# Kernel optimization log

Measured on AMD Instinct MI355X. Metric: run time of the kernel, lower is better.

The kernel has to match this reference:

```python
import jax, jax.numpy as jnp
import numpy as np

B, I, H, O = 64, 2048, 2048, 2048


def setup_inputs() -> dict:
    key = jax.random.key(0)
    ks = jax.random.split(key, 17)
    s = 0.02  # keep activations in a sane range
    return {
        "x": jax.random.normal(ks[0], (B, I), jnp.float32),
        "h_prev": jax.random.normal(ks[1], (B, H), jnp.float32),
        "c_prev": jax.random.normal(ks[2], (B, H), jnp.float32),
        "Wfh": jax.random.normal(ks[3], (H, H), jnp.float32) * s,
        "Wfx": jax.random.normal(ks[4], (I, H), jnp.float32) * s,
        "bf": jax.random.normal(ks[5], (H,), jnp.float32) * s,
        "Wih": jax.random.normal(ks[6], (H, H), jnp.float32) * s,
        "Wix": jax.random.normal(ks[7], (I, H), jnp.float32) * s,
        "bi": jax.random.normal(ks[8], (H,), jnp.float32) * s,
        "Woh": jax.random.normal(ks[9], (H, H), jnp.float32) * s,
        "Wox": jax.random.normal(ks[10], (I, H), jnp.float32) * s,
        "bo": jax.random.normal(ks[11], (H,), jnp.float32) * s,
        "Wch": jax.random.normal(ks[12], (H, H), jnp.float32) * s,
        "Wcx": jax.random.normal(ks[13], (I, H), jnp.float32) * s,
        "bc": jax.random.normal(ks[14], (H,), jnp.float32) * s,
        "Wy": jax.random.normal(ks[15], (H, O), jnp.float32) * s,
        "by": jax.random.normal(ks[16], (O,), jnp.float32) * s,
    }


def reference(x, h_prev, c_prev, Wfh, Wfx, bf, Wih, Wix, bi,
              Woh, Wox, bo, Wch, Wcx, bc, Wy, by):
    # Fused single-step LSTM cell: concat the 4 per-gate matmuls into
    # two GEMMs ([B,H]@[H,4H] and [B,I]@[I,4H]) -- same math as the
    # original 8 separate matmuls, gate order (f, i, c~, o).
    Wh = jnp.concatenate([Wfh, Wih, Wch, Woh], axis=1)  # [H, 4H]
    Wx = jnp.concatenate([Wfx, Wix, Wcx, Wox], axis=1)  # [I, 4H]
    b = jnp.concatenate([bf, bi, bc, bo], axis=0)       # [4H]
    gates = h_prev @ Wh + x @ Wx + b                     # [B, 4H]
    f_, i_, ct_, o_ = jnp.split(gates, 4, axis=1)
    f = jax.nn.sigmoid(f_)
    i = jax.nn.sigmoid(i_)
    ct = jnp.tanh(ct_)
    o = jax.nn.sigmoid(o_)
    c = f * c_prev + i * ct
    h = o * jnp.tanh(c)
    # NOTE: original computes y from the PREVIOUS hidden state (hList[-1])
    y = h_prev @ Wy + by
    # Pack (y, h_new, c_new) along feature dim (O == H) for a single output.
    return jnp.concatenate([y, h, c], axis=-1)  # [B, O + 2H]
```

## Files before the change

### kernel.cpp

```cpp
#include <hip/hip_runtime.h>

#define GAS __attribute__((address_space(1)))
#define LAS __attribute__((address_space(3)))

typedef short  bf16x8  __attribute__((ext_vector_type(8)));
typedef float  f32x4   __attribute__((ext_vector_type(4)));
typedef float  f32x16  __attribute__((ext_vector_type(16)));
typedef unsigned short ushort;

__device__ __forceinline__ short f2bf(float f) {
  __bf16 h = (__bf16)f;
  return __builtin_bit_cast(short, h);
}

#define GATE_PART 0
#define Y_PART    4194304
#define ABF_OFF   5242880

__global__ __launch_bounds__(256) void lstm_aconv(
    const float* __restrict__ X, const float* __restrict__ H,
    ushort* __restrict__ Abf)
{
  const int t  = blockIdx.x * 256 + threadIdx.x;
  const int e0 = t * 8;
  const int b  = e0 >> 12;
  const int k  = e0 & 4095;
  const float* src = (k < 2048) ? (H + (size_t)b * 2048 + k)
                                : (X + (size_t)b * 2048 + (k - 2048));
  f32x4 v0 = *(const f32x4*)(src);
  f32x4 v1 = *(const f32x4*)(src + 4);
  bf16x8 o;
  o[0] = f2bf(v0[0]); o[1] = f2bf(v0[1]); o[2] = f2bf(v0[2]); o[3] = f2bf(v0[3]);
  o[4] = f2bf(v1[0]); o[5] = f2bf(v1[1]); o[6] = f2bf(v1[2]); o[7] = f2bf(v1[3]);
  *(bf16x8*)(Abf + e0) = o;
}

__global__ __launch_bounds__(256, 2) void lstm_gemm(
    const float* __restrict__ Wfh, const float* __restrict__ Wfx, const float* __restrict__ bfp,
    const float* __restrict__ Wih, const float* __restrict__ Wix, const float* __restrict__ bip,
    const float* __restrict__ Woh, const float* __restrict__ Wox, const float* __restrict__ bop,
    const float* __restrict__ Wch, const float* __restrict__ Wcx, const float* __restrict__ bcp,
    const float* __restrict__ Wy,  const float* __restrict__ by,
    float* __restrict__ ws)
{
  __shared__ float  ldsW[2][64 * 128];
  __shared__ ushort ldsA[2][64 * 64];

  const int tid  = threadIdx.x;
  const int lane = tid & 63;
  const int widx = tid >> 6;
  const int n    = lane & 31;
  const int kg8  = (lane >> 5) << 3;
  const int j0w  = widx * 32;
  const ushort* Abf = (const ushort*)(ws + ABF_OFF);

  const int bid = blockIdx.x;
  const float* Wmat; int krow0m, aK0, nch;
  float bias; float* outBase; int outStride;

  if (bid < 512) {
    const int gate   = bid >> 7;
    const int stripe = (bid >> 3) & 15;
    const int ks     = bid & 7;
    const int j0     = stripe * 128;
    const float *Wg_h, *Wg_x, *bg;
    if      (gate == 0) { Wg_h = Wfh; Wg_x = Wfx; bg = bfp; }
    else if (gate == 1) { Wg_h = Wih; Wg_x = Wix; bg = bip; }
    else if (gate == 2) { Wg_h = Wch; Wg_x = Wcx; bg = bcp; }
    else                { Wg_h = Woh; Wg_x = Wox; bg = bop; }
    Wmat    = ((ks < 4) ? Wg_h : Wg_x) + j0;
    krow0m  = (ks & 3) * 512;
    aK0     = ks * 512;
    nch     = 8;
    bias    = (ks == 0) ? bg[j0 + j0w + n] : 0.f;
    outBase = ws + GATE_PART + (size_t)ks * 524288 + (size_t)gate * 2048 + j0 + j0w + n;
    outStride = 8192;
  } else {
    const int yi     = bid - 512;
    const int stripe = yi >> 3;
    const int ksy    = yi & 7;
    const int j0     = stripe * 128;
    Wmat    = Wy + j0;
    krow0m  = ksy * 256;
    aK0     = krow0m;
    nch     = 4;
    bias    = (ksy == 0) ? by[j0 + j0w + n] : 0.f;
    outBase = ws + Y_PART + (size_t)ksy * 131072 + j0 + j0w + n;
    outStride = 2048;
  }

  auto stageW = [&](int buf, int krow) {
    #pragma unroll
    for (int i = 0; i < 8; ++i) {
      const int r = i * 8 + widx * 2 + (lane >> 5);
      const float* src = Wmat + (size_t)(krow + r) * 2048 + (lane & 31) * 4;
      float* dst = &ldsW[buf][(i * 8 + widx * 2) * 128];
      __builtin_amdgcn_global_load_lds((const GAS unsigned*)src,
                                       (LAS unsigned*)dst, 16, 0, 0);
    }
  };
  auto stageA = [&](int buf, int aK) {
    #pragma unroll
    for (int i = 0; i < 2; ++i) {
      const int b    = i * 32 + widx * 8 + (lane >> 3);
      const int coff = (((lane & 7) * 16) ^ ((b & 7) << 4)) >> 1;
      const ushort* src = Abf + (size_t)b * 4096 + aK + coff;
      ushort* dst = &ldsA[buf][(i * 32 + widx * 8) * 64];
      __builtin_amdgcn_global_load_lds((const GAS unsigned*)src,
                                       (LAS unsigned*)dst, 16, 0, 0);
    }
  };

  f32x16 acc0, acc1;
  #pragma unroll
  for (int r = 0; r < 16; ++r) { acc0[r] = bias; acc1[r] = bias; }

  stageW(0, krow0m); stageA(0, aK0);

  for (int ch = 0; ch < nch; ++ch) {
    if (ch + 1 < nch) {
      stageW((ch + 1) & 1, krow0m + (ch + 1) * 64);
      stageA((ch + 1) & 1, aK0 + (ch + 1) * 64);
      asm volatile("s_waitcnt vmcnt(10)" ::: "memory");
    } else {
      asm volatile("s_waitcnt vmcnt(0)" ::: "memory");
    }
    __builtin_amdgcn_s_barrier();

    {
      const int buf = ch & 1;
      const char* ab = (const char*)&ldsA[buf][0];
      #pragma unroll
      for (int k0 = 0; k0 < 64; k0 += 16) {
        const int kk = k0 + kg8;
        float wf[8];
        #pragma unroll
        for (int i = 0; i < 8; ++i)
          wf[i] = ldsW[buf][(kk + i) * 128 + j0w + n];
        bf16x8 bfrag;
        #pragma unroll
        for (int i = 0; i < 8; ++i) bfrag[i] = f2bf(wf[i]);
        bf16x8 a0 = *(const bf16x8*)(ab + (((n)      * 128 + kk * 2) ^ ((n & 7) << 4)));
        bf16x8 a1 = *(const bf16x8*)(ab + (((n + 32) * 128 + kk * 2) ^ ((n & 7) << 4)));
        acc0 = __builtin_amdgcn_mfma_f32_32x32x16_bf16(a0, bfrag, acc0, 0, 0, 0);
        acc1 = __builtin_amdgcn_mfma_f32_32x32x16_bf16(a1, bfrag, acc1, 0, 0, 0);
      }
    }
    __builtin_amdgcn_s_barrier();
  }

  const int rbase = 4 * (lane >> 5);
  #pragma unroll
  for (int r = 0; r < 16; ++r) {
    const int row = (r & 3) + 8 * (r >> 2) + rbase;
    outBase[(size_t)row * outStride]        = acc0[r];
    outBase[(size_t)(row + 32) * outStride] = acc1[r];
  }
}

__device__ __forceinline__ float fsigmoid(float x) {
  return 1.f / (1.f + __expf(-x));
}
__device__ __forceinline__ float ftanh(float x) {
  return 1.f - 2.f / (1.f + __expf(2.f * x));
}

__global__ __launch_bounds__(64) void lstm_combine(
    const float* __restrict__ ws, const float* __restrict__ c_prev,
    float* __restrict__ out)
{
  const int t  = blockIdx.x * 64 + threadIdx.x;
  const int b  = t >> 9;
  const int j4 = (t & 511) * 4;

  f32x4 g[4];
  #pragma unroll
  for (int gg = 0; gg < 4; ++gg) {
    f32x4 s = (f32x4){0.f, 0.f, 0.f, 0.f};
    #pragma unroll
    for (int ks = 0; ks < 8; ++ks)
      s += *(const f32x4*)(ws + GATE_PART + (size_t)ks * 524288 + (size_t)b * 8192 + gg * 2048 + j4);
    g[gg] = s;
  }
  f32x4 ysum = (f32x4){0.f, 0.f, 0.f, 0.f};
  #pragma unroll
  for (int ks = 0; ks < 8; ++ks)
    ysum += *(const f32x4*)(ws + Y_PART + (size_t)ks * 131072 + (size_t)b * 2048 + j4);

  const f32x4 cp = *(const f32x4*)(c_prev + (size_t)b * 2048 + j4);
  f32x4 hF, cF;
  #pragma unroll
  for (int e = 0; e < 4; ++e) {
    float f  = fsigmoid(g[0][e]);
    float i  = fsigmoid(g[1][e]);
    float ct = ftanh(g[2][e]);
    float o  = fsigmoid(g[3][e]);
    float c  = f * cp[e] + i * ct;
    cF[e] = c;
    hF[e] = o * ftanh(c);
  }
  float* ob = out + (size_t)b * 6144;
  *(f32x4*)(ob + j4)        = ysum;
  *(f32x4*)(ob + 2048 + j4) = hF;
  *(f32x4*)(ob + 4096 + j4) = cF;
}

extern "C" void kernel_launch(void* const* d_in, const int* in_sizes, int n_in,
                              void* d_out, int out_size, void* d_ws, size_t ws_size,
                              hipStream_t stream)
{
  const float* X   = (const float*)d_in[0];
  const float* H   = (const float*)d_in[1];
  const float* Cp  = (const float*)d_in[2];
  const float* Wfh = (const float*)d_in[3];
  const float* Wfx = (const float*)d_in[4];
  const float* bfp = (const float*)d_in[5];
  const float* Wih = (const float*)d_in[6];
  const float* Wix = (const float*)d_in[7];
  const float* bip = (const float*)d_in[8];
  const float* Woh = (const float*)d_in[9];
  const float* Wox = (const float*)d_in[10];
  const float* bop = (const float*)d_in[11];
  const float* Wch = (const float*)d_in[12];
  const float* Wcx = (const float*)d_in[13];
  const float* bcp = (const float*)d_in[14];
  const float* Wy  = (const float*)d_in[15];
  const float* by  = (const float*)d_in[16];
  float* ws  = (float*)d_ws;
  float* out = (float*)d_out;

  lstm_aconv<<<128, 256, 0, stream>>>(X, H, (ushort*)(ws + ABF_OFF));
  lstm_gemm<<<640, 256, 0, stream>>>(Wfh, Wfx, bfp, Wih, Wix, bip,
                                     Woh, Wox, bop, Wch, Wcx, bcp, Wy, by, ws);
  lstm_combine<<<512, 64, 0, stream>>>(ws, Cp, out);
}
```

Measured before the change: 203.2 us.

## Stage weights as bf16 in LDS via registers, load A directly from global

Replaces the async global-to-LDS copy of fp32 weights with register loads that convert to bf16 before writing a padded LDS tile. This halves LDS footprint and moves the conversion out of the MFMA inner loop. A fragments are now read straight from global memory instead of staged through LDS, and occupancy is raised to 4 blocks per CU. The register prefetch of the next chunk overlaps with the MFMAs. The risks are more register pressure, uncoalesced A loads from global, and one barrier per chunk.

Measured after the change: 206.2 us. No clear change (+1.5%).

```diff
diff --git a/kernel.cpp b/kernel.cpp
--- a/kernel.cpp
+++ b/kernel.cpp
@@ -1,21 +1,20 @@
 #include <hip/hip_runtime.h>
-
-#define GAS __attribute__((address_space(1)))
-#define LAS __attribute__((address_space(3)))
 
 typedef short  bf16x8  __attribute__((ext_vector_type(8)));
 typedef float  f32x4   __attribute__((ext_vector_type(4)));
 typedef float  f32x16  __attribute__((ext_vector_type(16)));
 typedef unsigned short ushort;
-
-__device__ __forceinline__ short f2bf(float f) {
+typedef unsigned short u16x4 __attribute__((ext_vector_type(4)));
+
+__device__ __forceinline__ ushort f2bf(float f) {
   __bf16 h = (__bf16)f;
-  return __builtin_bit_cast(short, h);
+  return (ushort)__builtin_bit_cast(unsigned short, h);
 }
 
 #define GATE_PART 0
 #define Y_PART    4194304
 #define ABF_OFF   5242880
+#define WBUF      8448
 
 __global__ __launch_bounds__(256) void lstm_aconv(
     const float* __restrict__ X, const float* __restrict__ H,
@@ -30,12 +29,101 @@
   f32x4 v0 = *(const f32x4*)(src);
   f32x4 v1 = *(const f32x4*)(src + 4);
   bf16x8 o;
-  o[0] = f2bf(v0[0]); o[1] = f2bf(v0[1]); o[2] = f2bf(v0[2]); o[3] = f2bf(v0[3]);
-  o[4] = f2bf(v1[0]); o[5] = f2bf(v1[1]); o[6] = f2bf(v1[2]); o[7] = f2bf(v1[3]);
+  o[0] = (short)f2bf(v0[0]); o[1] = (short)f2bf(v0[1]);
+  o[2] = (short)f2bf(v0[2]); o[3] = (short)f2bf(v0[3]);
+  o[4] = (short)f2bf(v1[0]); o[5] = (short)f2bf(v1[1]);
+  o[6] = (short)f2bf(v1[2]); o[7] = (short)f2bf(v1[3]);
   *(bf16x8*)(Abf + e0) = o;
 }
 
-__global__ __launch_bounds__(256, 2) void lstm_gemm(
+template<int NCH>
+__device__ __forceinline__ void gemm_job(
+    const float* __restrict__ Wm, int krow0,
+    const ushort* __restrict__ Ap0,
+    float bias, float* __restrict__ outBase, int outStride,
+    ushort* __restrict__ ldsW, int lane, int widx)
+{
+  const int n    = lane & 31;
+  const int kg8  = (lane >> 5) << 3;
+  const int rsub = widx * 2 + (lane >> 5);
+  const int c0   = (lane & 31) * 4;
+  const int j0w  = widx * 32;
+  const ushort* Ap1 = Ap0 + (size_t)32 * 4096;
+
+  f32x16 acc0, acc1;
+  #pragma unroll
+  for (int r = 0; r < 16; ++r) { acc0[r] = bias; acc1[r] = bias; }
+
+  {
+    f32x4 w[8];
+    #pragma unroll
+    for (int i = 0; i < 8; ++i)
+      w[i] = *(const f32x4*)(Wm + (size_t)(krow0 + i * 8 + rsub) * 2048 + c0);
+    #pragma unroll
+    for (int i = 0; i < 8; ++i) {
+      u16x4 u;
+      #pragma unroll
+      for (int j = 0; j < 4; ++j) u[j] = f2bf(w[i][j]);
+      *(u16x4*)(ldsW + (i * 8 + rsub) * 132 + c0) = u;
+    }
+    __syncthreads();
+  }
+
+  #pragma unroll
+  for (int ch = 0; ch < NCH; ++ch) {
+    const ushort* lw = ldsW + (ch & 1) * WBUF;
+
+    bf16x8 a0[4], a1[4];
+    #pragma unroll
+    for (int k0 = 0; k0 < 4; ++k0) {
+      a0[k0] = *(const bf16x8*)(Ap0 + ch * 64 + k0 * 16 + kg8);
+      a1[k0] = *(const bf16x8*)(Ap1 + ch * 64 + k0 * 16 + kg8);
+    }
+    __builtin_amdgcn_sched_barrier(0);
+
+    f32x4 w[8];
+    if (ch + 1 < NCH) {
+      #pragma unroll
+      for (int i = 0; i < 8; ++i)
+        w[i] = *(const f32x4*)(Wm + (size_t)(krow0 + (ch + 1) * 64 + i * 8 + rsub) * 2048 + c0);
+    }
+    __builtin_amdgcn_sched_barrier(0);
+
+    #pragma unroll
+    for (int k0 = 0; k0 < 4; ++k0) {
+      const int kk = k0 * 16 + kg8;
+      bf16x8 bfrag;
+      #pragma unroll
+      for (int i = 0; i < 8; ++i)
+        bfrag[i] = (short)lw[(kk + i) * 132 + j0w + n];
+      acc0 = __builtin_amdgcn_mfma_f32_32x32x16_bf16(a0[k0], bfrag, acc0, 0, 0, 0);
+      acc1 = __builtin_amdgcn_mfma_f32_32x32x16_bf16(a1[k0], bfrag, acc1, 0, 0, 0);
+    }
+    __builtin_amdgcn_sched_barrier(0);
+
+    if (ch + 1 < NCH) {
+      ushort* dst = ldsW + ((ch & 1) ^ 1) * WBUF;
+      #pragma unroll
+      for (int i = 0; i < 8; ++i) {
+        u16x4 u;
+        #pragma unroll
+        for (int j = 0; j < 4; ++j) u[j] = f2bf(w[i][j]);
+        *(u16x4*)(dst + (i * 8 + rsub) * 132 + c0) = u;
+      }
+      __syncthreads();
+    }
+  }
+
+  const int rbase = 4 * (lane >> 5);
+  #pragma unroll
+  for (int r = 0; r < 16; ++r) {
+    const int row = (r & 3) + 8 * (r >> 2) + rbase;
+    outBase[(size_t)row * outStride]        = acc0[r];
+    outBase[(size_t)(row + 32) * outStride] = acc1[r];
+  }
+}
+
+__global__ __launch_bounds__(256, 4) void lstm_gemm(
     const float* __restrict__ Wfh, const float* __restrict__ Wfx, const float* __restrict__ bfp,
     const float* __restrict__ Wih, const float* __restrict__ Wix, const float* __restrict__ bip,
     const float* __restrict__ Woh, const float* __restrict__ Wox, const float* __restrict__ bop,
@@ -43,20 +131,15 @@
     const float* __restrict__ Wy,  const float* __restrict__ by,
     float* __restrict__ ws)
 {
-  __shared__ float  ldsW[2][64 * 128];
-  __shared__ ushort ldsA[2][64 * 64];
+  __shared__ ushort ldsW[2 * WBUF];
 
   const int tid  = threadIdx.x;
   const int lane = tid & 63;
   const int widx = tid >> 6;
   const int n    = lane & 31;
-  const int kg8  = (lane >> 5) << 3;
   const int j0w  = widx * 32;
   const ushort* Abf = (const ushort*)(ws + ABF_OFF);
-
   const int bid = blockIdx.x;
-  const float* Wmat; int krow0m, aK0, nch;
-  float bias; float* outBase; int outStride;
 
   if (bid < 512) {
     const int gate   = bid >> 7;
@@ -68,93 +151,24 @@
     else if (gate == 1) { Wg_h = Wih; Wg_x = Wix; bg = bip; }
     else if (gate == 2) { Wg_h = Wch; Wg_x = Wcx; bg = bcp; }
     else                { Wg_h = Woh; Wg_x = Wox; bg = bop; }
-    Wmat    = ((ks < 4) ? Wg_h : Wg_x) + j0;
-    krow0m  = (ks & 3) * 512;
-    aK0     = ks * 512;
-    nch     = 8;
-    bias    = (ks == 0) ? bg[j0 + j0w + n] : 0.f;
-    outBase = ws + GATE_PART + (size_t)ks * 524288 + (size_t)gate * 2048 + j0 + j0w + n;
-    outStride = 8192;
+    const float* Wm  = ((ks < 4) ? Wg_h : Wg_x) + j0;
+    const int krow0  = (ks & 3) * 512;
+    const int aK0    = ks * 512;
+    const float bias = (ks == 0) ? bg[j0 + j0w + n] : 0.f;
+    float* outBase = ws + GATE_PART + (size_t)ks * 524288 + (size_t)gate * 2048 + j0 + j0w + n;
+    const ushort* Ap0 = Abf + (size_t)n * 4096 + aK0;
+    gemm_job<8>(Wm, krow0, Ap0, bias, outBase, 8192, ldsW, lane, widx);
   } else {
     const int yi     = bid - 512;
     const int stripe = yi >> 3;
     const int ksy    = yi & 7;
     const int j0     = stripe * 128;
-    Wmat    = Wy + j0;
-    krow0m  = ksy * 256;
-    aK0     = krow0m;
-    nch     = 4;
-    bias    = (ksy == 0) ? by[j0 + j0w + n] : 0.f;
-    outBase = ws + Y_PART + (size_t)ksy * 131072 + j0 + j0w + n;
-    outStride = 2048;
-  }
-
-  auto stageW = [&](int buf, int krow) {
-    #pragma unroll
-    for (int i = 0; i < 8; ++i) {
-      const int r = i * 8 + widx * 2 + (lane >> 5);
-      const float* src = Wmat + (size_t)(krow + r) * 2048 + (lane & 31) * 4;
-      float* dst = &ldsW[buf][(i * 8 + widx * 2) * 128];
-      __builtin_amdgcn_global_load_lds((const GAS unsigned*)src,
-                                       (LAS unsigned*)dst, 16, 0, 0);
-    }
-  };
-  auto stageA = [&](int buf, int aK) {
-    #pragma unroll
-    for (int i = 0; i < 2; ++i) {
-      const int b    = i * 32 + widx * 8 + (lane >> 3);
-      const int coff = (((lane & 7) * 16) ^ ((b & 7) << 4)) >> 1;
-      const ushort* src = Abf + (size_t)b * 4096 + aK + coff;
-      ushort* dst = &ldsA[buf][(i * 32 + widx * 8) * 64];
-      __builtin_amdgcn_global_load_lds((const GAS unsigned*)src,
-                                       (LAS unsigned*)dst, 16, 0, 0);
-    }
-  };
-
-  f32x16 acc0, acc1;
-  #pragma unroll
-  for (int r = 0; r < 16; ++r) { acc0[r] = bias; acc1[r] = bias; }
-
-  stageW(0, krow0m); stageA(0, aK0);
-
-  for (int ch = 0; ch < nch; ++ch) {
-    if (ch + 1 < nch) {
-      stageW((ch + 1) & 1, krow0m + (ch + 1) * 64);
-      stageA((ch + 1) & 1, aK0 + (ch + 1) * 64);
-      asm volatile("s_waitcnt vmcnt(10)" ::: "memory");
-    } else {
-      asm volatile("s_waitcnt vmcnt(0)" ::: "memory");
-    }
-    __builtin_amdgcn_s_barrier();
-
-    {
-      const int buf = ch & 1;
-      const char* ab = (const char*)&ldsA[buf][0];
-      #pragma unroll
-      for (int k0 = 0; k0 < 64; k0 += 16) {
-        const int kk = k0 + kg8;
-        float wf[8];
-        #pragma unroll
-        for (int i = 0; i < 8; ++i)
-          wf[i] = ldsW[buf][(kk + i) * 128 + j0w + n];
-        bf16x8 bfrag;
-        #pragma unroll
-        for (int i = 0; i < 8; ++i) bfrag[i] = f2bf(wf[i]);
-        bf16x8 a0 = *(const bf16x8*)(ab + (((n)      * 128 + kk * 2) ^ ((n & 7) << 4)));
-        bf16x8 a1 = *(const bf16x8*)(ab + (((n + 32) * 128 + kk * 2) ^ ((n & 7) << 4)));
-        acc0 = __builtin_amdgcn_mfma_f32_32x32x16_bf16(a0, bfrag, acc0, 0, 0, 0);
-        acc1 = __builtin_amdgcn_mfma_f32_32x32x16_bf16(a1, bfrag, acc1, 0, 0, 0);
-      }
-    }
-    __builtin_amdgcn_s_barrier();
-  }
-
-  const int rbase = 4 * (lane >> 5);
-  #pragma unroll
-  for (int r = 0; r < 16; ++r) {
-    const int row = (r & 3) + 8 * (r >> 2) + rbase;
-    outBase[(size_t)row * outStride]        = acc0[r];
-    outBase[(size_t)(row + 32) * outStride] = acc1[r];
+    const float* Wm  = Wy + j0;
+    const int krow0  = ksy * 256;
+    const float bias = (ksy == 0) ? by[j0 + j0w + n] : 0.f;
+    float* outBase = ws + Y_PART + (size_t)ksy * 131072 + j0 + j0w + n;
+    const ushort* Ap0 = Abf + (size_t)n * 4096 + krow0;
+    gemm_job<4>(Wm, krow0, Ap0, bias, outBase, 2048, ldsW, lane, widx);
   }
 }
 
```

## Fold Wy GEMM into gate blocks and deepen pipeline to four stages

Applied to the files above, without the earlier changes.

Drops the separate 128 Wy blocks and gives the first 128 gate blocks a 24-chunk job that finishes the gate GEMM and then the Wy slice, so the grid shrinks from 640 to 512 blocks. The K-chunk is halved to 32 and staging uses a 4-buffer ring with three chunks in flight instead of double buffering, aiming to hide more global-load latency. The A tile swizzle is removed, which may bring LDS bank conflicts. The 128 longer blocks may add a tail that erases the benefit of fewer blocks.

After: 204.9 us. Within noise of the previous version (+0.8%).

```diff
diff --git a/kernel.cpp b/kernel.cpp
--- a/kernel.cpp
+++ b/kernel.cpp
@@ -8,9 +8,9 @@
 typedef float  f32x16  __attribute__((ext_vector_type(16)));
 typedef unsigned short ushort;
 
-__device__ __forceinline__ short f2bf(float f) {
+__device__ __forceinline__ ushort f2bf(float f) {
   __bf16 h = (__bf16)f;
-  return __builtin_bit_cast(short, h);
+  return __builtin_bit_cast(unsigned short, h);
 }
 
 #define GATE_PART 0
@@ -30,9 +30,104 @@
   f32x4 v0 = *(const f32x4*)(src);
   f32x4 v1 = *(const f32x4*)(src + 4);
   bf16x8 o;
-  o[0] = f2bf(v0[0]); o[1] = f2bf(v0[1]); o[2] = f2bf(v0[2]); o[3] = f2bf(v0[3]);
-  o[4] = f2bf(v1[0]); o[5] = f2bf(v1[1]); o[6] = f2bf(v1[2]); o[7] = f2bf(v1[3]);
+  o[0] = (short)f2bf(v0[0]); o[1] = (short)f2bf(v0[1]);
+  o[2] = (short)f2bf(v0[2]); o[3] = (short)f2bf(v0[3]);
+  o[4] = (short)f2bf(v1[0]); o[5] = (short)f2bf(v1[1]);
+  o[6] = (short)f2bf(v1[2]); o[7] = (short)f2bf(v1[3]);
   *(bf16x8*)(Abf + e0) = o;
+}
+
+template<int NCC>
+__device__ __forceinline__ void gemm_job(
+    const float* __restrict__ Wg,  int krow0g, int aK0g,
+    const float* __restrict__ Wyb, int yk0,
+    float biasG, float biasY,
+    float* __restrict__ outG, float* __restrict__ outY,
+    const ushort* __restrict__ Abf,
+    float* __restrict__ ldsW, ushort* __restrict__ ldsA,
+    int lane, int widx)
+{
+  const int n   = lane & 31;
+  const int kg8 = (lane >> 5) << 3;
+  const int j0w = widx * 32;
+
+  auto stage = [&](int cc) {
+    const int buf = cc & 3;
+    const float* wsM; int krow, aK;
+    if (cc < 16) { wsM = Wg;  krow = krow0g + cc * 32;        aK = aK0g + cc * 32; }
+    else         { wsM = Wyb; krow = yk0 + (cc - 16) * 32;    aK = yk0  + (cc - 16) * 32; }
+    #pragma unroll
+    for (int i = 0; i < 4; ++i) {
+      const float* src = wsM + (size_t)(krow + i * 8 + widx * 2 + (lane >> 5)) * 2048
+                             + (lane & 31) * 4;
+      float* dst = ldsW + (size_t)buf * 4096 + (i * 8 + widx * 2) * 128;
+      __builtin_amdgcn_global_load_lds((const GAS unsigned*)src,
+                                       (LAS unsigned*)dst, 16, 0, 0);
+    }
+    {
+      const ushort* src = Abf + (size_t)(widx * 16 + (lane >> 2)) * 4096 + aK
+                              + (lane & 3) * 8;
+      ushort* dst = ldsA + (size_t)buf * 2048 + widx * 16 * 32;
+      __builtin_amdgcn_global_load_lds((const GAS unsigned*)src,
+                                       (LAS unsigned*)dst, 16, 0, 0);
+    }
+  };
+
+  f32x16 acc0, acc1;
+  #pragma unroll
+  for (int r = 0; r < 16; ++r) { acc0[r] = biasG; acc1[r] = biasG; }
+
+  auto writeOut = [&](float* base, int stride) {
+    const int rbase = 4 * (lane >> 5);
+    #pragma unroll
+    for (int r = 0; r < 16; ++r) {
+      const int row = (r & 3) + 8 * (r >> 2) + rbase;
+      base[(size_t)row * stride]        = acc0[r];
+      base[(size_t)(row + 32) * stride] = acc1[r];
+    }
+  };
+
+  stage(0); stage(1); stage(2);
+
+  #pragma unroll
+  for (int cc = 0; cc < NCC; ++cc) {
+    if (cc + 3 < NCC) stage(cc + 3);
+    const int rem = NCC - 1 - cc;
+    if      (rem >= 3) asm volatile("s_waitcnt vmcnt(15)" ::: "memory");
+    else if (rem == 2) asm volatile("s_waitcnt vmcnt(10)" ::: "memory");
+    else if (rem == 1) asm volatile("s_waitcnt vmcnt(5)"  ::: "memory");
+    else               asm volatile("s_waitcnt vmcnt(0)"  ::: "memory");
+    __builtin_amdgcn_s_barrier();
+
+    {
+      const float*  lw = ldsW + (size_t)(cc & 3) * 4096;
+      const ushort* la = ldsA + (size_t)(cc & 3) * 2048;
+      #pragma unroll
+      for (int k0 = 0; k0 < 32; k0 += 16) {
+        const int kk = k0 + kg8;
+        float wf[8];
+        #pragma unroll
+        for (int i = 0; i < 8; ++i)
+          wf[i] = lw[(kk + i) * 128 + j0w + n];
+        bf16x8 bfrag;
+        #pragma unroll
+        for (int i = 0; i < 8; ++i) bfrag[i] = (short)f2bf(wf[i]);
+        bf16x8 a0 = *(const bf16x8*)(la + (size_t)n * 32 + kk);
+        bf16x8 a1 = *(const bf16x8*)(la + (size_t)(n + 32) * 32 + kk);
+        acc0 = __builtin_amdgcn_mfma_f32_32x32x16_bf16(a0, bfrag, acc0, 0, 0, 0);
+        acc1 = __builtin_amdgcn_mfma_f32_32x32x16_bf16(a1, bfrag, acc1, 0, 0, 0);
+      }
+    }
+    if (NCC > 16 && cc == 15) {
+      writeOut(outG, 8192);
+      #pragma unroll
+      for (int r = 0; r < 16; ++r) { acc0[r] = biasY; acc1[r] = biasY; }
+    }
+    __builtin_amdgcn_s_barrier();
+  }
+
+  if (NCC > 16) writeOut(outY, 2048);
+  else          writeOut(outG, 8192);
 }
 
 __global__ __launch_bounds__(256, 2) void lstm_gemm(
@@ -43,118 +138,45 @@
     const float* __restrict__ Wy,  const float* __restrict__ by,
     float* __restrict__ ws)
 {
-  __shared__ float  ldsW[2][64 * 128];
-  __shared__ ushort ldsA[2][64 * 64];
+  __shared__ float  ldsW[4 * 32 * 128];
+  __shared__ ushort ldsA[4 * 64 * 32];
 
   const int tid  = threadIdx.x;
   const int lane = tid & 63;
   const int widx = tid >> 6;
   const int n    = lane & 31;
-  const int kg8  = (lane >> 5) << 3;
   const int j0w  = widx * 32;
   const ushort* Abf = (const ushort*)(ws + ABF_OFF);
 
-  const int bid = blockIdx.x;
-  const float* Wmat; int krow0m, aK0, nch;
-  float bias; float* outBase; int outStride;
-
-  if (bid < 512) {
-    const int gate   = bid >> 7;
-    const int stripe = (bid >> 3) & 15;
-    const int ks     = bid & 7;
-    const int j0     = stripe * 128;
-    const float *Wg_h, *Wg_x, *bg;
-    if      (gate == 0) { Wg_h = Wfh; Wg_x = Wfx; bg = bfp; }
-    else if (gate == 1) { Wg_h = Wih; Wg_x = Wix; bg = bip; }
-    else if (gate == 2) { Wg_h = Wch; Wg_x = Wcx; bg = bcp; }
-    else                { Wg_h = Woh; Wg_x = Wox; bg = bop; }
-    Wmat    = ((ks < 4) ? Wg_h : Wg_x) + j0;
-    krow0m  = (ks & 3) * 512;
-    aK0     = ks * 512;
-    nch     = 8;
-    bias    = (ks == 0) ? bg[j0 + j0w + n] : 0.f;
-    outBase = ws + GATE_PART + (size_t)ks * 524288 + (size_t)gate * 2048 + j0 + j0w + n;
-    outStride = 8192;
+  const int bid    = blockIdx.x;
+  const int gate   = bid >> 7;
+  const int gs     = bid & 127;
+  const int stripe = gs >> 3;
+  const int ks     = gs & 7;
+  const int j0     = stripe * 128;
+
+  const float *Wg_h, *Wg_x, *bg;
+  if      (gate == 0) { Wg_h = Wfh; Wg_x = Wfx; bg = bfp; }
+  else if (gate == 1) { Wg_h = Wih; Wg_x = Wix; bg = bip; }
+  else if (gate == 2) { Wg_h = Wch; Wg_x = Wcx; bg = bcp; }
+  else                { Wg_h = Woh; Wg_x = Wox; bg = bop; }
+
+  const float* Wg    = ((ks < 4) ? Wg_h : Wg_x) + j0;
+  const int    krow0 = (ks & 3) * 512;
+  const int    aK0   = ks * 512;
+  const float  biasG = (ks == 0) ? bg[j0 + j0w + n] : 0.f;
+  float* outG = ws + GATE_PART + (size_t)ks * 524288 + (size_t)gate * 2048 + j0 + j0w + n;
+
+  if (bid < 128) {
+    const float* Wyb  = Wy + j0;
+    const int    yk0  = ks * 256;
+    const float  biasY = (ks == 0) ? by[j0 + j0w + n] : 0.f;
+    float* outY = ws + Y_PART + (size_t)ks * 131072 + j0 + j0w + n;
+    gemm_job<24>(Wg, krow0, aK0, Wyb, yk0, biasG, biasY, outG, outY,
+                 Abf, ldsW, ldsA, lane, widx);
   } else {
-    const int yi     = bid - 512;
-    const int stripe = yi >> 3;
-    const int ksy    = yi & 7;
-    const int j0     = stripe * 128;
-    Wmat    = Wy + j0;
-    krow0m  = ksy * 256;
-    aK0     = krow0m;
-    nch     = 4;
-    bias    = (ksy == 0) ? by[j0 + j0w + n] : 0.f;
-    outBase = ws + Y_PART + (size_t)ksy * 131072 + j0 + j0w + n;
-    outStride = 2048;
-  }
-
-  auto stageW = [&](int buf, int krow) {
-    #pragma unroll
-    for (int i = 0; i < 8; ++i) {
-      const int r = i * 8 + widx * 2 + (lane >> 5);
-      const float* src = Wmat + (size_t)(krow + r) * 2048 + (lane & 31) * 4;
-      float* dst = &ldsW[buf][(i * 8 + widx * 2) * 128];
-      __builtin_amdgcn_global_load_lds((const GAS unsigned*)src,
-                                       (LAS unsigned*)dst, 16, 0, 0);
-    }
-  };
-  auto stageA = [&](int buf, int aK) {
-    #pragma unroll
-    for (int i = 0; i < 2; ++i) {
-      const int b    = i * 32 + widx * 8 + (lane >> 3);
-      const int coff = (((lane & 7) * 16) ^ ((b & 7) << 4)) >> 1;
-      const ushort* src = Abf + (size_t)b * 4096 + aK + coff;
-      ushort* dst = &ldsA[buf][(i * 32 + widx * 8) * 64];
-      __builtin_amdgcn_global_load_lds((const GAS unsigned*)src,
-                                       (LAS unsigned*)dst, 16, 0, 0);
-    }
-  };
-
-  f32x16 acc0, acc1;
-  #pragma unroll
-  for (int r = 0; r < 16; ++r) { acc0[r] = bias; acc1[r] = bias; }
-
-  stageW(0, krow0m); stageA(0, aK0);
-
-  for (int ch = 0; ch < nch; ++ch) {
-    if (ch + 1 < nch) {
-      stageW((ch + 1) & 1, krow0m + (ch + 1) * 64);
-      stageA((ch + 1) & 1, aK0 + (ch + 1) * 64);
-      asm volatile("s_waitcnt vmcnt(10)" ::: "memory");
-    } else {
-      asm volatile("s_waitcnt vmcnt(0)" ::: "memory");
-    }
-    __builtin_amdgcn_s_barrier();
-
-    {
-      const int buf = ch & 1;
-      const char* ab = (const char*)&ldsA[buf][0];
-      #pragma unroll
-      for (int k0 = 0; k0 < 64; k0 += 16) {
-        const int kk = k0 + kg8;
-        float wf[8];
-        #pragma unroll
-        for (int i = 0; i < 8; ++i)
-          wf[i] = ldsW[buf][(kk + i) * 128 + j0w + n];
-        bf16x8 bfrag;
-        #pragma unroll
-        for (int i = 0; i < 8; ++i) bfrag[i] = f2bf(wf[i]);
-        bf16x8 a0 = *(const bf16x8*)(ab + (((n)      * 128 + kk * 2) ^ ((n & 7) << 4)));
-        bf16x8 a1 = *(const bf16x8*)(ab + (((n + 32) * 128 + kk * 2) ^ ((n & 7) << 4)));
-        acc0 = __builtin_amdgcn_mfma_f32_32x32x16_bf16(a0, bfrag, acc0, 0, 0, 0);
-        acc1 = __builtin_amdgcn_mfma_f32_32x32x16_bf16(a1, bfrag, acc1, 0, 0, 0);
-      }
-    }
-    __builtin_amdgcn_s_barrier();
-  }
-
-  const int rbase = 4 * (lane >> 5);
-  #pragma unroll
-  for (int r = 0; r < 16; ++r) {
-    const int row = (r & 3) + 8 * (r >> 2) + rbase;
-    outBase[(size_t)row * outStride]        = acc0[r];
-    outBase[(size_t)(row + 32) * outStride] = acc1[r];
+    gemm_job<16>(Wg, krow0, aK0, Wg, 0, biasG, 0.f, outG, outG,
+                 Abf, ldsW, ldsA, lane, widx);
   }
 }
 
@@ -230,7 +252,7 @@
   float* out = (float*)d_out;
 
   lstm_aconv<<<128, 256, 0, stream>>>(X, H, (ushort*)(ws + ABF_OFF));
-  lstm_gemm<<<640, 256, 0, stream>>>(Wfh, Wfx, bfp, Wih, Wix, bip,
+  lstm_gemm<<<512, 256, 0, stream>>>(Wfh, Wfx, bfp, Wih, Wix, bip,
                                      Woh, Wox, bop, Wch, Wcx, bcp, Wy, by, ws);
   lstm_combine<<<512, 64, 0, stream>>>(ws, Cp, out);
 }
```
